# Performance work log

Measured on AMD Instinct MI355X. Metric: run time of the kernel, lower is better.

The kernel has to match this reference:

```python
import jax, jax.numpy as jnp
import numpy as np

# sizes
No, Nc, Ns, Nn, Nd = 80000, 20000, 5000, 500, 50
H, L, C = 256, 3, 1024  # hidden_dim, num_layers, NUM_CLASSES (VOCAB_SIZE=1023)
OCC_F, CHORD_F, SEC_F, NOTE_F, SD_F = 64, 32, 16, 16, 8
EPS = 1e-5


def setup_inputs() -> dict:
    key = jax.random.key(0)
    ks = iter(jax.random.split(key, 64))

    def nrm(sh, s=0.05):
        return jax.random.normal(next(ks), sh, jnp.float32) * s

    def edge(n, hi_s, hi_d):
        s = jax.random.randint(next(ks), (n,), 0, hi_s, dtype=jnp.int32)
        d = jax.random.randint(next(ks), (n,), 0, hi_d, dtype=jnp.int32)
        return jnp.stack([s, d])

    inp = {
        'x_occ': nrm((No, OCC_F), 1.0), 'x_chord': nrm((Nc, CHORD_F), 1.0),
        'x_sec': nrm((Ns, SEC_F), 1.0), 'x_note': nrm((Nn, NOTE_F), 1.0),
        'x_sd': nrm((Nd, SD_F), 1.0),
        'ei_occ_occ': edge(No, No, No),
        'ei_occ_chord': edge(No, No, Nc),
        'ei_chord_occ': edge(No, Nc, No),
        'ei_occ_sec': edge(No, No, Ns),
        'ei_sec_occ': edge(No, Ns, No),
        'ei_sec_sec': edge(Ns, Ns, Ns),
        'ei_chord_note': edge(4 * Nc, Nc, Nn),
        'ei_note_chord': edge(4 * Nc, Nn, Nc),
        'ei_chord_sd': edge(Nc, Nc, Nd),
        'ei_sd_chord': edge(Nc, Nd, Nc),
        # type-specific input projections (torch Linear: y = x @ W.T + b)
        'W_occ': nrm((H, OCC_F + CHORD_F)), 'b_occ': jnp.zeros((H,), jnp.float32),
        'W_chord': nrm((H, CHORD_F)), 'b_chord': jnp.zeros((H,), jnp.float32),
        'W_sec': nrm((H, SEC_F)), 'b_sec': jnp.zeros((H,), jnp.float32),
        'W_note': nrm((H, NOTE_F)), 'b_note': jnp.zeros((H,), jnp.float32),
        'W_sd': nrm((H, SD_F)), 'b_sd': jnp.zeros((H,), jnp.float32),
        'type_emb': nrm((5, H)),
        # per-layer SAGEConv: lin_l (on aggregated, with bias) + lin_r (on root)
        'Wl': nrm((L, H, H)), 'bl': jnp.zeros((L, H), jnp.float32),
        'Wr': nrm((L, H, H)),
        'ln_g': jnp.ones((L, H), jnp.float32), 'ln_b': jnp.zeros((L, H), jnp.float32),
        'Wc': nrm((C, H)), 'bc': jnp.zeros((C,), jnp.float32),
    }
    return inp


def _forward(x_occ, x_chord, x_sec, x_note, x_sd,
             W_occ, b_occ, W_chord, b_chord, W_sec, b_sec, W_note, b_note,
             W_sd, b_sd, type_emb, Wl, bl, Wr, ln_g, ln_b, Wc, bc, edges):
    (ei_occ_occ, ei_occ_chord, ei_chord_occ, ei_occ_sec, ei_sec_occ,
     ei_sec_sec, ei_chord_note, ei_note_chord, ei_chord_sd, ei_sd_chord) = edges

    # enrich occ inputs with chord features via scatter-set over inst_rev edges
    chord_per_occ = jnp.zeros((No, CHORD_F), x_occ.dtype)
    chord_per_occ = chord_per_occ.at[ei_chord_occ[1]].set(x_chord[ei_chord_occ[0]])
    occ_in = jnp.concatenate([x_occ, chord_per_occ], axis=1)

    h = jnp.concatenate([
        occ_in @ W_occ.T + b_occ + type_emb[0],
        x_chord @ W_chord.T + b_chord + type_emb[1],
        x_sec @ W_sec.T + b_sec + type_emb[2],
        x_note @ W_note.T + b_note + type_emb[3],
        x_sd @ W_sd.T + b_sd + type_emb[4],
    ], axis=0)  # [N, H]
    N = No + Nc + Ns + Nn + Nd
    o_occ, o_chord, o_sec, o_note, o_sd = 0, No, No + Nc, No + Nc + Ns, No + Nc + Ns + Nn

    # concatenate homogeneous edge set with node-type offsets
    pairs = [(ei_occ_occ, o_occ, o_occ), (ei_occ_chord, o_occ, o_chord),
             (ei_chord_occ, o_chord, o_occ), (ei_occ_sec, o_occ, o_sec),
             (ei_sec_occ, o_sec, o_occ), (ei_sec_sec, o_sec, o_sec),
             (ei_chord_note, o_chord, o_note), (ei_note_chord, o_note, o_chord),
             (ei_chord_sd, o_chord, o_sd), (ei_sd_chord, o_sd, o_chord)]
    src = jnp.concatenate([ei[0] + a for ei, a, _ in pairs])
    dst = jnp.concatenate([ei[1] + b for ei, _, b in pairs])

    # mean in-degree normalizer (shared across layers)
    cnt = jax.ops.segment_sum(jnp.ones_like(dst, h.dtype), dst, num_segments=N)
    inv_cnt = (1.0 / jnp.maximum(cnt, 1.0))[:, None]  # [N, 1]

    for l in range(L):
        # SAGEConv: lin_l(mean_{j->i} h_j) + lin_r(h_i)
        agg = jax.ops.segment_sum(h[src], dst, num_segments=N) * inv_cnt
        conv = agg @ Wl[l].T + bl[l] + h @ Wr[l].T
        # LayerNorm (dropout is identity in eval) + residual
        mu = conv.mean(axis=-1, keepdims=True)
        xc = conv - mu
        var = (xc * xc).mean(axis=-1, keepdims=True)
        h = xc * jax.lax.rsqrt(var + EPS) * ln_g[l] + ln_b[l] + h

    return h[:No] @ Wc.T + bc  # [N_occ, NUM_CLASSES]


def reference(x_occ, x_chord, x_sec, x_note, x_sd,
              ei_occ_occ, ei_occ_chord, ei_chord_occ, ei_occ_sec, ei_sec_occ,
              ei_sec_sec, ei_chord_note, ei_note_chord, ei_chord_sd, ei_sd_chord,
              W_occ, b_occ, W_chord, b_chord, W_sec, b_sec, W_note, b_note,
              W_sd, b_sd, type_emb, Wl, bl, Wr, ln_g, ln_b, Wc, bc):
    edges = (ei_occ_occ, ei_occ_chord, ei_chord_occ, ei_occ_sec, ei_sec_occ,
             ei_sec_sec, ei_chord_note, ei_note_chord, ei_chord_sd, ei_sd_chord)
    return _forward(x_occ, x_chord, x_sec, x_note, x_sd,
                    W_occ, b_occ, W_chord, b_chord, W_sec, b_sec, W_note, b_note,
                    W_sd, b_sd, type_emb, Wl, bl, Wr, ln_g, ln_b, Wc, bc, edges)
```

## Files before the change

### kernel.cpp

```cpp
#include <hip/hip_runtime.h>


#define kNo 80000
#define kNc 20000
#define kNs 5000
#define kNn 500
#define kNd 50
#define kN  105550
#define kH  256
#define kC  1024
#define kE  605000
#define LN_EPS 1e-5f
#define NBLK 413

typedef unsigned int u32;
typedef unsigned short ush;
typedef __attribute__((ext_vector_type(8))) short short8;
typedef __attribute__((ext_vector_type(4))) float f32x4;

__device__ __forceinline__ float b2f(ush b) {
  u32 u = ((u32)b) << 16;
  float f;
  __builtin_memcpy(&f, &u, 4);
  return f;
}
__device__ __forceinline__ ush f2b(float x) {
  u32 u;
  __builtin_memcpy(&u, &x, 4);
  u32 r = (u + 0x7fffu + ((u >> 16) & 1u)) >> 16;
  return (ush)r;
}
__device__ __forceinline__ float up_hi(u32 u) {
  u32 v = u & 0xffff0000u;
  float f;
  __builtin_memcpy(&f, &v, 4);
  return f;
}
__device__ __forceinline__ float up_lo(u32 u) {
  u32 v = u << 16;
  float f;
  __builtin_memcpy(&f, &v, 4);
  return f;
}
__device__ __forceinline__ float upk(u32 u) { return up_hi(u) + up_lo(u); }
__device__ __forceinline__ u32 pk(float x) {
  ush hi = f2b(x);
  ush lo = f2b(x - b2f(hi));
  return (((u32)hi) << 16) | (u32)lo;
}

union S8u {
  u32 w[4];
  short8 s;
};
__device__ __forceinline__ void unpk8(uint4 a, uint4 b, short8& hi, short8& lo) {
  S8u h, l;
  h.w[0] = (a.x >> 16) | (a.y & 0xffff0000u);
  h.w[1] = (a.z >> 16) | (a.w & 0xffff0000u);
  h.w[2] = (b.x >> 16) | (b.y & 0xffff0000u);
  h.w[3] = (b.z >> 16) | (b.w & 0xffff0000u);
  l.w[0] = (a.x & 0xffffu) | (a.y << 16);
  l.w[1] = (a.z & 0xffffu) | (a.w << 16);
  l.w[2] = (b.x & 0xffffu) | (b.y << 16);
  l.w[3] = (b.z & 0xffffu) | (b.w << 16);
  hi = h.s;
  lo = l.s;
}

__device__ __forceinline__ void gload16(const void* g, void* l) {
  __builtin_amdgcn_global_load_lds((const __attribute__((address_space(1))) u32*)g,
                                   (__attribute__((address_space(3))) u32*)l, 16, 0, 0);
}

struct EdgeTab {
  const int* p[10];
  int n[10], so[10], dofs[10], cum[11];
};

__global__ __launch_bounds__(256) void k_edges(EdgeTab t, int* __restrict__ src_g,
                                               int* __restrict__ dst_g,
                                               int* __restrict__ cnt) {
  int e = blockIdx.x * 256 + threadIdx.x;
  if (e >= kE) return;
  int s = 0;
#pragma unroll
  for (int i = 1; i < 10; ++i) s += (e >= t.cum[i]) ? 1 : 0;
  int j = e - t.cum[s];
  const int* p = t.p[s];
  int src = p[j] + t.so[s];
  int dst = p[t.n[s] + j] + t.dofs[s];
  src_g[e] = src;
  dst_g[e] = dst;
  atomicAdd(&cnt[dst], 1);
}

__global__ __launch_bounds__(256) void k_winner(const int* __restrict__ ei,
                                                int* __restrict__ winner) {
  int e = blockIdx.x * 256 + threadIdx.x;
  if (e >= kNo) return;
  atomicMax(&winner[ei[kNo + e]], e);
}

__global__ __launch_bounds__(256) void k_scat(const int* __restrict__ ei,
                                              const int* __restrict__ winner,
                                              const float* __restrict__ xch,
                                              float* __restrict__ cpo) {
  int tid = blockIdx.x * 256 + threadIdx.x;
  if (tid >= kNo * 8) return;
  int e = tid >> 3, q = tid & 7;
  int d = ei[kNo + e];
  if (winner[d] == e) {
    int s = ei[e];
    ((float4*)cpo)[d * 8 + q] = ((const float4*)xch)[s * 8 + q];
  }
}

__global__ __launch_bounds__(256) void k_pack2(const float* __restrict__ A1, int K1,
                                               const float* __restrict__ A2, int K2,
                                               int Kp, u32* __restrict__ Xp, int M) {
  int tid = blockIdx.x * 256 + threadIdx.x;
  if (tid >= M * Kp) return;
  int r = tid / Kp, c = tid - r * Kp;
  float v = 0.f;
  if (c < K1) v = A1[(size_t)r * K1 + c];
  else if (c < K1 + K2) v = A2[(size_t)r * K2 + (c - K1)];
  Xp[tid] = pk(v);
}

__global__ __launch_bounds__(256) void k_wsplit(const float* __restrict__ W, int K,
                                                int Kp, ush* __restrict__ hi,
                                                ush* __restrict__ lo) {
  int tid = blockIdx.x * 256 + threadIdx.x;
  if (tid >= 256 * Kp) return;
  int r = tid / Kp, c = tid - r * Kp;
  float v = (c < K) ? W[(size_t)r * K + c] : 0.f;
  ush h = f2b(v);
  hi[tid] = h;
  lo[tid] = f2b(v - b2f(h));
}

struct PArgs {
  const u32* Xp;
  const ush* Wh;
  const ush* Wlo;
  const float* bias;
  const float* emb;
  u32* out;
  int M, Kp;
};

__global__ __launch_bounds__(256) void k_pmg(PArgs g) {
  __shared__ u32 Apk[64 * 32];
  __shared__ ush Wht[256 * 32];
  __shared__ ush Wlt[256 * 32];

  const int tid = threadIdx.x;
  const int wv = tid >> 6;
  const int l = tid & 63;
  const int fr = l & 15, fk = l >> 4;
  const int r0 = blockIdx.x * 64;

  const int ac0 = (((fk * 2) ^ (fr & 7)) * 4);
  const int ac1 = (((fk * 2 + 1) ^ (fr & 7)) * 4);
  const int wc8 = ((fk ^ (fr & 3)) * 8);

  const int arow = tid >> 3, ach = tid & 7;
  const int wrow = tid >> 2, wch = tid & 3;
  const int ar0g = (r0 + arow < g.M) ? (r0 + arow) : (g.M - 1);
  const int ar1g = (r0 + arow + 32 < g.M) ? (r0 + arow + 32) : (g.M - 1);
  const int aswz = (ach ^ (arow & 7)) * 4;
  const int wswz = (wch ^ (wrow & 3)) * 8;

  f32x4 acc[4][4];
#pragma unroll
  for (int m = 0; m < 4; ++m)
#pragma unroll
    for (int n = 0; n < 4; ++n) acc[m][n] = (f32x4)(0.f);

  const u32* a0 = g.Xp + (size_t)ar0g * g.Kp + aswz;
  const u32* a1 = g.Xp + (size_t)ar1g * g.Kp + aswz;
  const ush* wh = g.Wh + (size_t)wrow * g.Kp + wswz;
  const ush* wl = g.Wlo + (size_t)wrow * g.Kp + wswz;

#pragma unroll 1
  for (int kc = 0; kc < g.Kp; kc += 32) {
    __syncthreads();
    gload16(a0 + kc, Apk + tid * 4);
    gload16(a1 + kc, Apk + (tid + 256) * 4);
#pragma unroll
    for (int i = 0; i < 4; ++i) {
      gload16(wh + (size_t)i * 64 * g.Kp + kc, Wht + (tid + i * 256) * 8);
      gload16(wl + (size_t)i * 64 * g.Kp + kc, Wlt + (tid + i * 256) * 8);
    }
    __syncthreads();

    short8 ah[4], al[4], whf[4], wlf[4];
#pragma unroll
    for (int m = 0; m < 4; ++m) {
      const uint4 x = *(const uint4*)(Apk + (m * 16 + fr) * 32 + ac0);
      const uint4 y = *(const uint4*)(Apk + (m * 16 + fr) * 32 + ac1);
      unpk8(x, y, ah[m], al[m]);
    }
#pragma unroll
    for (int n = 0; n < 4; ++n) {
      whf[n] = *(const short8*)(Wht + (wv * 64 + n * 16 + fr) * 32 + wc8);
      wlf[n] = *(const short8*)(Wlt + (wv * 64 + n * 16 + fr) * 32 + wc8);
    }
#pragma unroll
    for (int m = 0; m < 4; ++m)
#pragma unroll
      for (int n = 0; n < 4; ++n) {
        acc[m][n] = __builtin_amdgcn_mfma_f32_16x16x32_bf16(ah[m], whf[n],
                                                            acc[m][n], 0, 0, 0);
        acc[m][n] = __builtin_amdgcn_mfma_f32_16x16x32_bf16(ah[m], wlf[n],
                                                            acc[m][n], 0, 0, 0);
        acc[m][n] = __builtin_amdgcn_mfma_f32_16x16x32_bf16(al[m], whf[n],
                                                            acc[m][n], 0, 0, 0);
      }
  }

  float bn[4];
#pragma unroll
  for (int n = 0; n < 4; ++n) {
    const int col = wv * 64 + n * 16 + fr;
    bn[n] = g.bias[col] + g.emb[col];
  }
#pragma unroll
  for (int m = 0; m < 4; ++m)
#pragma unroll
    for (int j = 0; j < 4; ++j) {
      const int ri = r0 + m * 16 + fk * 4 + j;
      if (ri < g.M) {
        u32* op = g.out + (size_t)ri * kH + wv * 64 + fr;
#pragma unroll
        for (int n = 0; n < 4; ++n) op[n * 16] = pk(acc[m][n][j] + bn[n]);
      }
    }
}

__global__ __launch_bounds__(256) void k_scan1(const int* __restrict__ cnt,
                                               int* __restrict__ bsum) {
  __shared__ int s[256];
  int b = blockIdx.x, t = threadIdx.x;
  int i = b * 256 + t;
  s[t] = (i < kN) ? cnt[i] : 0;
  __syncthreads();
  for (int off = 128; off; off >>= 1) {
    if (t < off) s[t] += s[t + off];
    __syncthreads();
  }
  if (t == 0) bsum[b] = s[0];
}

__global__ __launch_bounds__(512) void k_scan2(const int* __restrict__ bsum,
                                               int* __restrict__ bscan) {
  __shared__ int s[512];
  int t = threadIdx.x;
  s[t] = (t < NBLK) ? bsum[t] : 0;
  __syncthreads();
  for (int off = 1; off < 512; off <<= 1) {
    int v = (t >= off) ? s[t - off] : 0;
    __syncthreads();
    s[t] += v;
    __syncthreads();
  }
  if (t < NBLK) bscan[t] = s[t];
}

__global__ __launch_bounds__(256) void k_scan3(const int* __restrict__ cnt,
                                               const int* __restrict__ bscan,
                                               int* __restrict__ rowptr,
                                               int* __restrict__ cursor,
                                               float* __restrict__ inv) {
  __shared__ int s[256];
  int b = blockIdx.x, t = threadIdx.x;
  int i = b * 256 + t;
  int v = (i < kN) ? cnt[i] : 0;
  s[t] = v;
  __syncthreads();
  for (int off = 1; off < 256; off <<= 1) {
    int u = (t >= off) ? s[t - off] : 0;
    __syncthreads();
    s[t] += u;
    __syncthreads();
  }
  int incl = s[t];
  int base = (b > 0) ? bscan[b - 1] : 0;
  int excl = base + incl - v;
  if (i < kN) {
    rowptr[i] = excl;
    cursor[i] = excl;
    inv[i] = 1.f / (float)(v > 1 ? v : 1);
    if (i == kN - 1) rowptr[kN] = excl + v;
  }
}

__global__ __launch_bounds__(256) void k_fill(const int* __restrict__ src_g,
                                              const int* __restrict__ dst_g,
                                              int* __restrict__ cursor,
                                              int* __restrict__ csr_src) {
  int e = blockIdx.x * 256 + threadIdx.x;
  if (e >= kE) return;
  int d = dst_g[e];
  int slot = atomicAdd(&cursor[d], 1);
  csr_src[slot] = src_g[e];
}

__global__ __launch_bounds__(256) void k_agg(const u32* __restrict__ hpk,
                                             const int* __restrict__ rowptr,
                                             const int* __restrict__ csr_src,
                                             const float* __restrict__ inv,
                                             u32* __restrict__ apk) {
  const int wave = threadIdx.x >> 6, lane = threadIdx.x & 63;
  const int node = kN - 1 - (blockIdx.x * 4 + wave);
  if (node < 0) return;
  const int jb = rowptr[node], je = rowptr[node + 1];
  float a0 = 0.f, a1 = 0.f, a2 = 0.f, a3 = 0.f;
  const int coff = lane * 4;

  int j = jb;
  while (j < je) {
    const int batch = min(je - j, 64);
    const int myi = csr_src[j + ((lane < batch) ? lane : (batch - 1))];
#pragma unroll 1
    for (int t0 = 0; t0 < batch; t0 += 8) {
      int s[8];
#pragma unroll
      for (int q = 0; q < 8; ++q) {
        const int tt = t0 + q;
        s[q] = __shfl(myi, (tt < batch) ? tt : 0);
      }
      uint4 v[8];
#pragma unroll
      for (int q = 0; q < 8; ++q)
        v[q] = *(const uint4*)(hpk + (size_t)s[q] * kH + coff);
#pragma unroll
      for (int q = 0; q < 8; ++q) {
        const bool ok = (t0 + q) < batch;
        a0 += ok ? upk(v[q].x) : 0.f;
        a1 += ok ? upk(v[q].y) : 0.f;
        a2 += ok ? upk(v[q].z) : 0.f;
        a3 += ok ? upk(v[q].w) : 0.f;
      }
    }
    j += batch;
  }
  const float ic = inv[node];
  uint4 o;
  o.x = pk(a0 * ic);
  o.y = pk(a1 * ic);
  o.z = pk(a2 * ic);
  o.w = pk(a3 * ic);
  *(uint4*)(apk + (size_t)node * kH + coff) = o;
}

struct GArgs {
  const u32* A[2];
  const ush* Wh[2];
  const ush* Wl[2];
  const float* bias;
  const float* lng;
  const float* lnb;
  const u32* rpk;
  float* outf;
  u32* opk;
  int M, npass, ostride;
};

template <bool LN>
__global__ __launch_bounds__(256) void k_mg(GArgs g) {
  __shared__ u32 Apk[64 * 32];
  __shared__ ush Wht[256 * 32];
  __shared__ ush Wlt[256 * 32];
  __shared__ float redS[4][64];
  __shared__ float redQ[4][64];

  const int tid = threadIdx.x;
  const int wv = tid >> 6;
  const int l = tid & 63;
  const int fr = l & 15, fk = l >> 4;

  int bx, by;
  if (LN) {
    bx = blockIdx.x;
    by = 0;
  } else {
    const int w = (blockIdx.x & 7) * 625 + (blockIdx.x >> 3);
    bx = w >> 2;
    by = w & 3;
  }
  const int r0 = bx * 64;
  const int cb = by << 8;

  const int ac0 = (((fk * 2) ^ (fr & 7)) * 4);
  const int ac1 = (((fk * 2 + 1) ^ (fr & 7)) * 4);
  const int wc8 = ((fk ^ ((fr >> 1) & 3)) * 8);

  const int arow = tid >> 3;
  const int ach = tid & 7;
  const int wrow = tid >> 2;
  const int wch = tid & 3;
  const int ar0g = (r0 + arow < g.M) ? (r0 + arow) : (g.M - 1);
  const int ar1g = (r0 + arow + 32 < g.M) ? (r0 + arow + 32) : (g.M - 1);
  const int aswz = (ach ^ (arow & 7)) * 4;
  const int wswz = (wch ^ ((wrow >> 1) & 3)) * 8;

  f32x4 acc[4][4];
#pragma unroll
  for (int m = 0; m < 4; ++m)
#pragma unroll
    for (int n = 0; n < 4; ++n) acc[m][n] = (f32x4)(0.f);

#pragma unroll 1
  for (int p = 0; p < g.npass; ++p) {
    const u32* a0 = g.A[p] + (size_t)ar0g * kH + aswz;
    const u32* a1 = g.A[p] + (size_t)ar1g * kH + aswz;
    const ush* wh = g.Wh[p] + (size_t)(cb + wrow) * kH + wswz;
    const ush* wl = g.Wl[p] + (size_t)(cb + wrow) * kH + wswz;
#pragma unroll 1
    for (int kc = 0; kc < kH; kc += 32) {
      __syncthreads();
      gload16(a0 + kc, Apk + tid * 4);
      gload16(a1 + kc, Apk + (tid + 256) * 4);
#pragma unroll
      for (int i = 0; i < 4; ++i) {
        gload16(wh + (size_t)i * 64 * kH + kc, Wht + (tid + i * 256) * 8);
        gload16(wl + (size_t)i * 64 * kH + kc, Wlt + (tid + i * 256) * 8);
      }
      __syncthreads();

      short8 ah[4], al[4], whf[4], wlf[4];
#pragma unroll
      for (int m = 0; m < 4; ++m) {
        const uint4 x = *(const uint4*)(Apk + (m * 16 + fr) * 32 + ac0);
        const uint4 y = *(const uint4*)(Apk + (m * 16 + fr) * 32 + ac1);
        unpk8(x, y, ah[m], al[m]);
      }
#pragma unroll
      for (int n = 0; n < 4; ++n) {
        whf[n] = *(const short8*)(Wht + (wv * 64 + n * 16 + fr) * 32 + wc8);
        wlf[n] = *(const short8*)(Wlt + (wv * 64 + n * 16 + fr) * 32 + wc8);
      }
#pragma unroll
      for (int m = 0; m < 4; ++m)
#pragma unroll
        for (int n = 0; n < 4; ++n) {
          acc[m][n] = __builtin_amdgcn_mfma_f32_16x16x32_bf16(ah[m], whf[n],
                                                              acc[m][n], 0, 0, 0);
          acc[m][n] = __builtin_amdgcn_mfma_f32_16x16x32_bf16(ah[m], wlf[n],
                                                              acc[m][n], 0, 0, 0);
          acc[m][n] = __builtin_amdgcn_mfma_f32_16x16x32_bf16(al[m], whf[n],
                                                              acc[m][n], 0, 0, 0);
        }
    }
  }

  float bn[4];
#pragma unroll
  for (int n = 0; n < 4; ++n) bn[n] = g.bias[cb + wv * 64 + n * 16 + fr];
#pragma unroll
  for (int m = 0; m < 4; ++m)
#pragma unroll
    for (int n = 0; n < 4; ++n)
#pragma unroll
      for (int j = 0; j < 4; ++j) acc[m][n][j] += bn[n];

  if (LN) {
#pragma unroll
    for (int m = 0; m < 4; ++m)
#pragma unroll
      for (int j = 0; j < 4; ++j) {
        float s = acc[m][0][j] + acc[m][1][j] + acc[m][2][j] + acc[m][3][j];
        float q = acc[m][0][j] * acc[m][0][j] + acc[m][1][j] * acc[m][1][j] +
                  acc[m][2][j] * acc[m][2][j] + acc[m][3][j] * acc[m][3][j];
#pragma unroll
        for (int d = 1; d < 16; d <<= 1) {
          s += __shfl_xor(s, d);
          q += __shfl_xor(q, d);
        }
        if (fr == 0) {
          redS[wv][m * 16 + fk * 4 + j] = s;
          redQ[wv][m * 16 + fk * 4 + j] = q;
        }
      }
    __syncthreads();
    float gg[4], eb[4];
#pragma unroll
    for (int n = 0; n < 4; ++n) {
      gg[n] = g.lng[wv * 64 + n * 16 + fr];
      eb[n] = g.lnb[wv * 64 + n * 16 + fr];
    }
#pragma unroll
    for (int m = 0; m < 4; ++m)
#pragma unroll
      for (int j = 0; j < 4; ++j) {
        const int rt = m * 16 + fk * 4 + j;
        const float S = redS[0][rt] + redS[1][rt] + redS[2][rt] + redS[3][rt];
        const float Q = redQ[0][rt] + redQ[1][rt] + redQ[2][rt] + redQ[3][rt];
        const float mu = S * (1.f / 256.f);
        float var = Q * (1.f / 256.f) - mu * mu;
        var = var > 0.f ? var : 0.f;
        const float rstd = rsqrtf(var + LN_EPS);
        const int ri = r0 + rt;
        if (ri < g.M) {
          const size_t base = (size_t)ri * kH + wv * 64 + fr;
#pragma unroll
          for (int n = 0; n < 4; ++n) {
            const size_t ix = base + n * 16;
            const float res = upk(g.rpk[ix]);
            const float y = (acc[m][n][j] - mu) * rstd * gg[n] + eb[n] + res;
            g.opk[ix] = pk(y);
          }
        }
      }
  } else {
#pragma unroll
    for (int m = 0; m < 4; ++m)
#pragma unroll
      for (int j = 0; j < 4; ++j) {
        const int ri = r0 + m * 16 + fk * 4 + j;
        if (ri < g.M) {
          float* op = g.outf + (size_t)ri * g.ostride + cb + wv * 64 + fr;
#pragma unroll
          for (int n = 0; n < 4; ++n) op[n * 16] = acc[m][n][j];
        }
      }
  }
}

__global__ __launch_bounds__(256) void k_split(const float* __restrict__ s,
                                               ush* __restrict__ hi,
                                               ush* __restrict__ lo, int n) {
  int i = blockIdx.x * 256 + threadIdx.x;
  if (i >= n) return;
  float v = s[i];
  ush h = f2b(v);
  hi[i] = h;
  lo[i] = f2b(v - b2f(h));
}

extern "C" void kernel_launch(void* const* d_in, const int* in_sizes, int n_in,
                              void* d_out, int out_size, void* d_ws, size_t ws_size,
                              hipStream_t stream) {
  (void)in_sizes; (void)n_in; (void)out_size; (void)ws_size;
  const float* x_occ    = (const float*)d_in[0];
  const float* x_chord  = (const float*)d_in[1];
  const float* x_sec    = (const float*)d_in[2];
  const float* x_note   = (const float*)d_in[3];
  const float* x_sd     = (const float*)d_in[4];
  const int* ei[10];
  for (int i = 0; i < 10; ++i) ei[i] = (const int*)d_in[5 + i];
  const float* W_occ    = (const float*)d_in[15];
  const float* b_occ    = (const float*)d_in[16];
  const float* W_chord  = (const float*)d_in[17];
  const float* b_chord  = (const float*)d_in[18];
  const float* W_sec    = (const float*)d_in[19];
  const float* b_sec    = (const float*)d_in[20];
  const float* W_note   = (const float*)d_in[21];
  const float* b_note   = (const float*)d_in[22];
  const float* W_sd     = (const float*)d_in[23];
  const float* b_sd     = (const float*)d_in[24];
  const float* type_emb = (const float*)d_in[25];
  const float* Wl       = (const float*)d_in[26];
  const float* bl       = (const float*)d_in[27];
  const float* Wr       = (const float*)d_in[28];
  const float* ln_g     = (const float*)d_in[29];
  const float* ln_b     = (const float*)d_in[30];
  const float* Wc       = (const float*)d_in[31];
  const float* bc       = (const float*)d_in[32];

  char* base = (char*)d_ws;
  u32* h_pk   = (u32*)(base);
  char* R = base + 108083200u;
  u32* agg_pk = (u32*)R;
  char* wb = base + 216166400u;
  ush* Wl_hi = (ush*)(wb);
  ush* Wl_lo = (ush*)(wb + 393216u);
  ush* Wr_hi = (ush*)(wb + 786432u);
  ush* Wr_lo = (ush*)(wb + 1179648u);
  ush* Wc_hi = (ush*)(wb + 1572864u);
  ush* Wc_lo = (ush*)(wb + 2097152u);
  ush* Wo_hi = (ush*)(wb + 2621440u);
  ush* Wo_lo = (ush*)(wb + 2670592u);
  ush* Wch_hi = (ush*)(wb + 2719744u);
  ush* Wch_lo = (ush*)(wb + 2736128u);
  ush* Wse_hi = (ush*)(wb + 2752512u);
  ush* Wse_lo = (ush*)(wb + 2768896u);
  ush* Wnt_hi = (ush*)(wb + 2785280u);
  ush* Wnt_lo = (ush*)(wb + 2801664u);
  ush* Wsd_hi = (ush*)(wb + 2818048u);
  ush* Wsd_lo = (ush*)(wb + 2834432u);
  int* ip = (int*)(wb + 2850816u);
  int* csr_src = ip;
  int* cnt     = ip + 605000;
  int* rowptr  = ip + 710550;
  int* cursor  = ip + 816101;
  float* inv   = (float*)(ip + 921651);
  int* bsum    = ip + 1027201;
  int* bscan   = ip + 1027614;
  float* cpo  = (float*)(R);
  int* winner = (int*)(R + 10240000u);
  int* src_g  = (int*)(R + 10560000u);
  int* dst_g  = (int*)(R + 12980000u);
  u32* Xp_occ = (u32*)(R + 16000000u);
  u32* Xp_ch  = (u32*)(R + 46720000u);
  u32* Xp_se  = (u32*)(R + 49280000u);
  u32* Xp_nt  = (u32*)(R + 49920000u);
  u32* Xp_sd  = (u32*)(R + 49984000u);

  hipMemsetAsync(winner, 0xFF, kNo * 4, stream);
  hipMemsetAsync(cpo, 0, (size_t)kNo * 32 * 4, stream);
  hipMemsetAsync(cnt, 0, kN * 4, stream);

  k_split<<<768, 256, 0, stream>>>(Wl, Wl_hi, Wl_lo, 3 * kH * kH);
  k_split<<<768, 256, 0, stream>>>(Wr, Wr_hi, Wr_lo, 3 * kH * kH);
  k_split<<<1024, 256, 0, stream>>>(Wc, Wc_hi, Wc_lo, kC * kH);

  k_wsplit<<<(256 * 96 + 255) / 256, 256, 0, stream>>>(W_occ, 96, 96, Wo_hi, Wo_lo);
  k_wsplit<<<32, 256, 0, stream>>>(W_chord, 32, 32, Wch_hi, Wch_lo);
  k_wsplit<<<32, 256, 0, stream>>>(W_sec, 16, 32, Wse_hi, Wse_lo);
  k_wsplit<<<32, 256, 0, stream>>>(W_note, 16, 32, Wnt_hi, Wnt_lo);
  k_wsplit<<<32, 256, 0, stream>>>(W_sd, 8, 32, Wsd_hi, Wsd_lo);

  k_winner<<<(kNo + 255) / 256, 256, 0, stream>>>(ei[2], winner);
  k_scat<<<(kNo * 8) / 256, 256, 0, stream>>>(ei[2], winner, x_chord, cpo);

  k_pack2<<<(kNo * 96 + 255) / 256, 256, 0, stream>>>(x_occ, 64, cpo, 32, 96, Xp_occ, kNo);
  k_pack2<<<(kNc * 32 + 255) / 256, 256, 0, stream>>>(x_chord, 32, nullptr, 0, 32, Xp_ch, kNc);
  k_pack2<<<(kNs * 32 + 255) / 256, 256, 0, stream>>>(x_sec, 16, nullptr, 0, 32, Xp_se, kNs);
  k_pack2<<<(kNn * 32 + 255) / 256, 256, 0, stream>>>(x_note, 16, nullptr, 0, 32, Xp_nt, kNn);
  k_pack2<<<(kNd * 32 + 255) / 256, 256, 0, stream>>>(x_sd, 8, nullptr, 0, 32, Xp_sd, kNd);

  {
    PArgs p{};
    p.Xp = Xp_occ; p.Wh = Wo_hi; p.Wlo = Wo_lo; p.bias = b_occ;
    p.emb = type_emb + 0 * kH; p.out = h_pk; p.M = kNo; p.Kp = 96;
    k_pmg<<<(kNo + 63) / 64, 256, 0, stream>>>(p);
    p.Xp = Xp_ch; p.Wh = Wch_hi; p.Wlo = Wch_lo; p.bias = b_chord;
    p.emb = type_emb + 1 * kH; p.out = h_pk + (size_t)kNo * kH; p.M = kNc; p.Kp = 32;
    k_pmg<<<(kNc + 63) / 64, 256, 0, stream>>>(p);
    p.Xp = Xp_se; p.Wh = Wse_hi; p.Wlo = Wse_lo; p.bias = b_sec;
    p.emb = type_emb + 2 * kH; p.out = h_pk + (size_t)100000 * kH; p.M = kNs; p.Kp = 32;
    k_pmg<<<(kNs + 63) / 64, 256, 0, stream>>>(p);
    p.Xp = Xp_nt; p.Wh = Wnt_hi; p.Wlo = Wnt_lo; p.bias = b_note;
    p.emb = type_emb + 3 * kH; p.out = h_pk + (size_t)105000 * kH; p.M = kNn; p.Kp = 32;
    k_pmg<<<(kNn + 63) / 64, 256, 0, stream>>>(p);
    p.Xp = Xp_sd; p.Wh = Wsd_hi; p.Wlo = Wsd_lo; p.bias = b_sd;
    p.emb = type_emb + 4 * kH; p.out = h_pk + (size_t)105500 * kH; p.M = kNd; p.Kp = 32;
    k_pmg<<<(kNd + 63) / 64, 256, 0, stream>>>(p);
  }

  EdgeTab tab;
  const int ns_[10]  = {80000, 80000, 80000, 80000, 80000, 5000, 80000, 80000, 20000, 20000};
  const int sos_[10] = {0, 0, 80000, 0, 100000, 100000, 80000, 105000, 80000, 105500};
  const int dos_[10] = {0, 80000, 0, 100000, 0, 100000, 105000, 80000, 105500, 80000};
  int cum = 0;
  for (int i = 0; i < 10; ++i) {
    tab.p[i] = ei[i]; tab.n[i] = ns_[i]; tab.so[i] = sos_[i]; tab.dofs[i] = dos_[i];
    tab.cum[i] = cum; cum += ns_[i];
  }
  tab.cum[10] = cum;

  k_edges<<<(kE + 255) / 256, 256, 0, stream>>>(tab, src_g, dst_g, cnt);
  k_scan1<<<NBLK, 256, 0, stream>>>(cnt, bsum);
  k_scan2<<<1, 512, 0, stream>>>(bsum, bscan);
  k_scan3<<<NBLK, 256, 0, stream>>>(cnt, bscan, rowptr, cursor, inv);
  k_fill<<<(kE + 255) / 256, 256, 0, stream>>>(src_g, dst_g, cursor, csr_src);

  for (int l = 0; l < 3; ++l) {
    k_agg<<<(kN + 3) / 4, 256, 0, stream>>>(h_pk, rowptr, csr_src, inv, agg_pk);
    GArgs a{};
    const size_t off = (size_t)l * kH * kH;
    a.A[0] = agg_pk;      a.A[1] = h_pk;
    a.Wh[0] = Wl_hi + off; a.Wh[1] = Wr_hi + off;
    a.Wl[0] = Wl_lo + off; a.Wl[1] = Wr_lo + off;
    a.bias = bl + l * kH;
    a.lng = ln_g + l * kH;
    a.lnb = ln_b + l * kH;
    a.rpk = h_pk;
    a.outf = nullptr;
    a.opk = h_pk;
    a.M = kN; a.npass = 2; a.ostride = kH;
    k_mg<true><<<dim3((kN + 63) / 64, 1), 256, 0, stream>>>(a);
  }

  GArgs c{};
  c.A[0] = h_pk;
  c.Wh[0] = Wc_hi;
  c.Wl[0] = Wc_lo;
  c.bias = bc;
  c.rpk = nullptr;
  c.outf = (float*)d_out;
  c.opk = nullptr;
  c.M = kNo; c.npass = 1; c.ostride = kC;
  k_mg<false><<<(kNo / 64) * 4, 256, 0, stream>>>(c);
}
```

Measured before the change: 1.224 ms.

## Double-buffer LDS tiles in MFMA GEMM to overlap global loads with compute

The GEMM kernel's pass and k-chunk loops are flattened into a single tile loop. Its shared-memory A and W tiles are double-buffered, so the next tile is loaded while MFMAs run on the current one, and each iteration needs one barrier instead of two. The LayerNorm reduction scratch now reuses the A buffer to offset the doubled LDS. Launch bounds now ask for 2 blocks per CU, which could limit registers and cause spills, and the larger LDS footprint may reduce occupancy.

```diff
diff --git a/kernel.cpp b/kernel.cpp
--- a/kernel.cpp
+++ b/kernel.cpp
@@ -367,13 +367,30 @@
   int M, npass, ostride;
 };
 
+#define STAGE_MG(t, b)                                                        \
+  {                                                                           \
+    const int p_ = (t) >> 3;                                                  \
+    const int kc_ = ((t) & 7) * 32;                                           \
+    const u32* aP_ = g.A[p_];                                                 \
+    gload16(aP_ + (size_t)ar0g * kH + aswz + kc_, &Apk[b][tid * 4]);          \
+    gload16(aP_ + (size_t)ar1g * kH + aswz + kc_, &Apk[b][(tid + 256) * 4]);  \
+    const ush* wh_ = g.Wh[p_] + (size_t)(cb + wrow) * kH + wswz + kc_;        \
+    const ush* wl_ = g.Wl[p_] + (size_t)(cb + wrow) * kH + wswz + kc_;        \
+    gload16(wh_, &Wht[b][tid * 8]);                                           \
+    gload16(wh_ + (size_t)64 * kH, &Wht[b][(256 + tid) * 8]);                 \
+    gload16(wh_ + (size_t)128 * kH, &Wht[b][(512 + tid) * 8]);                \
+    gload16(wh_ + (size_t)192 * kH, &Wht[b][(768 + tid) * 8]);                \
+    gload16(wl_, &Wlt[b][tid * 8]);                                           \
+    gload16(wl_ + (size_t)64 * kH, &Wlt[b][(256 + tid) * 8]);                 \
+    gload16(wl_ + (size_t)128 * kH, &Wlt[b][(512 + tid) * 8]);                \
+    gload16(wl_ + (size_t)192 * kH, &Wlt[b][(768 + tid) * 8]);                \
+  }
+
 template <bool LN>
-__global__ __launch_bounds__(256) void k_mg(GArgs g) {
-  __shared__ u32 Apk[64 * 32];
-  __shared__ ush Wht[256 * 32];
-  __shared__ ush Wlt[256 * 32];
-  __shared__ float redS[4][64];
-  __shared__ float redQ[4][64];
+__global__ __launch_bounds__(256, 2) void k_mg(GArgs g) {
+  __shared__ u32 Apk[2][64 * 32];
+  __shared__ ush Wht[2][256 * 32];
+  __shared__ ush Wlt[2][256 * 32];
 
   const int tid = threadIdx.x;
   const int wv = tid >> 6;
@@ -411,48 +428,42 @@
 #pragma unroll
     for (int n = 0; n < 4; ++n) acc[m][n] = (f32x4)(0.f);
 
+  const int nt = g.npass * 8;
+
+  STAGE_MG(0, 0);
+  __syncthreads();
+
+  int buf = 0;
 #pragma unroll 1
-  for (int p = 0; p < g.npass; ++p) {
-    const u32* a0 = g.A[p] + (size_t)ar0g * kH + aswz;
-    const u32* a1 = g.A[p] + (size_t)ar1g * kH + aswz;
-    const ush* wh = g.Wh[p] + (size_t)(cb + wrow) * kH + wswz;
-    const ush* wl = g.Wl[p] + (size_t)(cb + wrow) * kH + wswz;
-#pragma unroll 1
-    for (int kc = 0; kc < kH; kc += 32) {
-      __syncthreads();
-      gload16(a0 + kc, Apk + tid * 4);
-      gload16(a1 + kc, Apk + (tid + 256) * 4);
-#pragma unroll
-      for (int i = 0; i < 4; ++i) {
-        gload16(wh + (size_t)i * 64 * kH + kc, Wht + (tid + i * 256) * 8);
-        gload16(wl + (size_t)i * 64 * kH + kc, Wlt + (tid + i * 256) * 8);
+  for (int t = 0; t < nt; ++t) {
+    if (t + 1 < nt) STAGE_MG(t + 1, buf ^ 1);
+
+    short8 ah[4], al[4], whf[4], wlf[4];
+#pragma unroll
+    for (int m = 0; m < 4; ++m) {
+      const uint4 x = *(const uint4*)(&Apk[buf][(m * 16 + fr) * 32 + ac0]);
+      const uint4 y = *(const uint4*)(&Apk[buf][(m * 16 + fr) * 32 + ac1]);
+      unpk8(x, y, ah[m], al[m]);
+    }
+#pragma unroll
+    for (int n = 0; n < 4; ++n) {
+      whf[n] = *(const short8*)(&Wht[buf][(wv * 64 + n * 16 + fr) * 32 + wc8]);
+      wlf[n] = *(const short8*)(&Wlt[buf][(wv * 64 + n * 16 + fr) * 32 + wc8]);
+    }
+#pragma unroll
+    for (int m = 0; m < 4; ++m)
+#pragma unroll
+      for (int n = 0; n < 4; ++n) {
+        acc[m][n] = __builtin_amdgcn_mfma_f32_16x16x32_bf16(ah[m], whf[n],
+                                                            acc[m][n], 0, 0, 0);
+        acc[m][n] = __builtin_amdgcn_mfma_f32_16x16x32_bf16(ah[m], wlf[n],
+                                                            acc[m][n], 0, 0, 0);
+        acc[m][n] = __builtin_amdgcn_mfma_f32_16x16x32_bf16(al[m], whf[n],
+                                                            acc[m][n], 0, 0, 0);
       }
-      __syncthreads();
-
-      short8 ah[4], al[4], whf[4], wlf[4];
-#pragma unroll
-      for (int m = 0; m < 4; ++m) {
-        const uint4 x = *(const uint4*)(Apk + (m * 16 + fr) * 32 + ac0);
-        const uint4 y = *(const uint4*)(Apk + (m * 16 + fr) * 32 + ac1);
-        unpk8(x, y, ah[m], al[m]);
-      }
-#pragma unroll
-      for (int n = 0; n < 4; ++n) {
-        whf[n] = *(const short8*)(Wht + (wv * 64 + n * 16 + fr) * 32 + wc8);
-        wlf[n] = *(const short8*)(Wlt + (wv * 64 + n * 16 + fr) * 32 + wc8);
-      }
-#pragma unroll
-      for (int m = 0; m < 4; ++m)
-#pragma unroll
-        for (int n = 0; n < 4; ++n) {
-          acc[m][n] = __builtin_amdgcn_mfma_f32_16x16x32_bf16(ah[m], whf[n],
-                                                              acc[m][n], 0, 0, 0);
-          acc[m][n] = __builtin_amdgcn_mfma_f32_16x16x32_bf16(ah[m], wlf[n],
-                                                              acc[m][n], 0, 0, 0);
-          acc[m][n] = __builtin_amdgcn_mfma_f32_16x16x32_bf16(al[m], whf[n],
-                                                              acc[m][n], 0, 0, 0);
-        }
-    }
+
+    __syncthreads();
+    buf ^= 1;
   }
 
   float bn[4];
@@ -466,6 +477,8 @@
       for (int j = 0; j < 4; ++j) acc[m][n][j] += bn[n];
 
   if (LN) {
+    float* redS = (float*)&Apk[0][0];
+    float* redQ = ((float*)&Apk[0][0]) + 256;
 #pragma unroll
     for (int m = 0; m < 4; ++m)
 #pragma unroll
@@ -479,8 +492,8 @@
           q += __shfl_xor(q, d);
         }
         if (fr == 0) {
-          redS[wv][m * 16 + fk * 4 + j] = s;
-          redQ[wv][m * 16 + fk * 4 + j] = q;
+          redS[wv * 64 + m * 16 + fk * 4 + j] = s;
+          redQ[wv * 64 + m * 16 + fk * 4 + j] = q;
         }
       }
     __syncthreads();
@@ -495,8 +508,8 @@
 #pragma unroll
       for (int j = 0; j < 4; ++j) {
         const int rt = m * 16 + fk * 4 + j;
-        const float S = redS[0][rt] + redS[1][rt] + redS[2][rt] + redS[3][rt];
-        const float Q = redQ[0][rt] + redQ[1][rt] + redQ[2][rt] + redQ[3][rt];
+        const float S = redS[rt] + redS[64 + rt] + redS[128 + rt] + redS[192 + rt];
+        const float Q = redQ[rt] + redQ[64 + rt] + redQ[128 + rt] + redQ[192 + rt];
         const float mu = S * (1.f / 256.f);
         float var = Q * (1.f / 256.f) - mu * mu;
         var = var > 0.f ? var : 0.f;
```

Result: no change. 1.229 ms (+0.4%).
